# Performance work log

Measured on AMD Instinct MI355X. Metric: run time of the kernel, lower is better.

Reference implementation:

```python
import jax, jax.numpy as jnp
import numpy as np

N_NODES = 128; TIME_DIM = 16; XYZ_DIM = 63; B = 2; V = 1024
_PARAM_SHAPES = {
    'ec1_w': (N_NODES, 72 + TIME_DIM, 64), 'ec1_b': (N_NODES, 64),
    'ec21_w': (N_NODES, 64, 8), 'ec21_b': (N_NODES, 8),
    'ec22_w': (N_NODES, 64, 8), 'ec22_b': (N_NODES, 8),
    'dc1_w': (N_NODES, 80, 64), 'dc1_b': (N_NODES, 64),
    'dc21_w': (N_NODES, 64, 32), 'dc21_b': (N_NODES, 32),
    'dc22_w': (N_NODES, 64, 3), 'dc22_b': (N_NODES, 3),
    'f1_w': (N_NODES, 32 + XYZ_DIM, 64), 'f1_b': (N_NODES, 64),
    'f2_w': (N_NODES, 64, 64), 'f2_b': (N_NODES, 64),
    'f3_w': (N_NODES, 64, 64), 'f3_b': (N_NODES, 64),
    'f4_w': (N_NODES, 64, 256), 'f4_b': (N_NODES, 256),
    'c1_w': (256, 64), 'c1_b': (64,),
    'c2_w': (64, 3), 'c2_b': (3,),
    'd1_w': (256, 1), 'd1_b': (1,),
}
_PNAMES = list(_PARAM_SHAPES.keys())


def setup_inputs():
    key = jax.random.key(0)
    kt, kp, kl, km, kb, kw = jax.random.split(key, 6)
    inp = {
        't_ped': jax.random.normal(kt, (B, TIME_DIM), dtype=jnp.float32),
        'pose': jax.random.normal(kp, (B, 72), dtype=jnp.float32),
        'local_coords': jax.random.normal(kl, (N_NODES, B, V, XYZ_DIM), dtype=jnp.float32),
        'mask': jax.random.randint(km, (N_NODES, B, V), 0, 2) > 0,
        'bweights': jax.random.uniform(kb, (N_NODES, B, V), dtype=jnp.float32),
    }
    for i, (name, shape) in enumerate(_PARAM_SHAPES.items()):
        inp[name] = jax.random.normal(jax.random.fold_in(kw, i), shape, dtype=jnp.float32) * 0.02
    return inp


def _forward(t_ped, pose, local_coords, bweights, mask, p):
    relu = jax.nn.relu
    # ---- encode: 128 per-node Linear(88->64), then ->8 heads (batched as one einsum) ----
    enc_in = jnp.concatenate([t_ped, pose], axis=-1)                                    # [B,88]
    net = relu(jnp.einsum('bi,nio->nbo', enc_in, p['ec1_w']) + p['ec1_b'][:, None, :])  # [n,B,64]
    mean = jnp.einsum('nbi,nio->nbo', net, p['ec21_w']) + p['ec21_b'][:, None, :]       # [n,B,8]
    std = jax.nn.sigmoid(jnp.einsum('nbi,nio->nbo', net, p['ec22_w']) + p['ec22_b'][:, None, :])
    z = mean  # eval mode: z = mean
    # ---- decode: per-node Linear(80->64) then ->32 (ei) and ->3 (delta) ----
    pose_n = jnp.broadcast_to(pose, (N_NODES,) + pose.shape)                            # [n,B,72]
    dec_in = jnp.concatenate([z, pose_n], axis=-1)                                      # [n,B,80]
    dnet = relu(jnp.einsum('nbi,nio->nbo', dec_in, p['dc1_w']) + p['dc1_b'][:, None, :])
    ei = jnp.einsum('nbi,nio->nbo', dnet, p['dc21_w']) + p['dc21_b'][:, None, :]        # [n,B,32]
    nodes_delta = jnp.einsum('nbi,nio->nbo', dnet, p['dc22_w']) + p['dc22_b'][:, None, :]
    # ---- Feature_field: grouped 1x1 conv (groups=128) == per-node MLP; mask/mark
    # pack-unpack in the original is equivalent to dense compute + zeroing non-hits ----
    ei_e = jnp.broadcast_to(ei[:, :, None, :], (N_NODES, B, V, ei.shape[-1]))
    x = jnp.concatenate([ei_e, local_coords], axis=-1)                                  # [n,B,V,95]
    h = relu(jnp.einsum('nbvi,nio->nbvo', x, p['f1_w']) + p['f1_b'][:, None, None, :])
    h = relu(jnp.einsum('nbvi,nio->nbvo', h, p['f2_w']) + p['f2_b'][:, None, None, :])
    h = relu(jnp.einsum('nbvi,nio->nbvo', h, p['f3_w']) + p['f3_b'][:, None, None, :])
    f = relu(jnp.einsum('nbvi,nio->nbvo', h, p['f4_w']) + p['f4_b'][:, None, None, :])  # [n,B,V,256]
    f = jnp.where(mask[..., None], f, jnp.zeros((), f.dtype))                           # f[~mask] = 0
    # ---- blend_feature ----
    bw = jnp.transpose(bweights, (1, 2, 0)) + 1e-7                                      # [B,V,n]
    bw = bw / jnp.sum(bw, axis=-1, keepdims=True)
    f_blend = jnp.einsum('nbvc,bvn->bvc', f, bw)                                        # [B,V,256]
    # ---- Nerf head ----
    netc = relu(f_blend @ p['c1_w'] + p['c1_b'])
    c = netc @ p['c2_w'] + p['c2_b']
    d = relu(f_blend @ p['d1_w'] + p['d1_b'])
    return c, d, ei, nodes_delta, mean, std


def reference(t_ped, pose, local_coords, mask, bweights, ec1_w, ec1_b, ec21_w, ec21_b, ec22_w, ec22_b, dc1_w, dc1_b, dc21_w, dc21_b, dc22_w, dc22_b, f1_w, f1_b, f2_w, f2_b, f3_w, f3_b, f4_w, f4_b, c1_w, c1_b, c2_w, c2_b, d1_w, d1_b):
    p = dict(zip(_PNAMES, (ec1_w, ec1_b, ec21_w, ec21_b, ec22_w, ec22_b, dc1_w, dc1_b, dc21_w, dc21_b, dc22_w, dc22_b, f1_w, f1_b, f2_w, f2_b, f3_w, f3_b, f4_w, f4_b, c1_w, c1_b, c2_w, c2_b, d1_w, d1_b)))
    return _forward(t_ped, pose, local_coords, bweights, mask, p)
```

## Files before the change

### kernel.cpp

```cpp
#include <hip/hip_runtime.h>
#include <hip/hip_bf16.h>
#include <math.h>

typedef __attribute__((ext_vector_type(8))) short short8;
typedef __attribute__((ext_vector_type(4))) float f32x4;

#define W1P_OFF   0u
#define W2P_OFF   1572864u
#define W3P_OFF   2621440u
#define W4P_OFF   3670016u
#define EI_OFF    7864320u
#define RECIP_OFF 7897088u
#define PART_OFF  7905280u

#define OUT_C    0
#define OUT_D    6144
#define OUT_EI   8192
#define OUT_ND   16384
#define OUT_MEAN 17152
#define OUT_STD  19200

__global__ void pack_weights(const float* __restrict__ f1w, const float* __restrict__ f2w,
                             const float* __restrict__ f3w, const float* __restrict__ f4w,
                             __hip_bfloat16* __restrict__ w1p, __hip_bfloat16* __restrict__ w2p,
                             __hip_bfloat16* __restrict__ w3p, __hip_bfloat16* __restrict__ w4p) {
  int id = blockIdx.x * 256 + threadIdx.x;
  union { __hip_bfloat16 h[8]; int4 v; } u;
  if (id < 98304) {
    int n = id / 768, r = id % 768, kc = r >> 6, o = r & 63;
    #pragma unroll
    for (int e = 0; e < 8; e++) {
      int k = kc * 8 + e;
      float val = (k < 95) ? f1w[((size_t)n * 95 + k) * 64 + o] : 0.f;
      u.h[e] = __float2bfloat16(val);
    }
    reinterpret_cast<int4*>(w1p)[id] = u.v;
  } else if (id < 163840) {
    int id2 = id - 98304;
    int n = id2 / 512, r = id2 % 512, kc = r >> 6, o = r & 63;
    #pragma unroll
    for (int e = 0; e < 8; e++)
      u.h[e] = __float2bfloat16(f2w[((size_t)n * 64 + kc * 8 + e) * 64 + o]);
    reinterpret_cast<int4*>(w2p)[id2] = u.v;
  } else if (id < 229376) {
    int id3 = id - 163840;
    int n = id3 / 512, r = id3 % 512, kc = r >> 6, o = r & 63;
    #pragma unroll
    for (int e = 0; e < 8; e++)
      u.h[e] = __float2bfloat16(f3w[((size_t)n * 64 + kc * 8 + e) * 64 + o]);
    reinterpret_cast<int4*>(w3p)[id3] = u.v;
  } else if (id < 491520) {
    int id4 = id - 229376;
    int n = id4 / 2048, r = id4 % 2048, kc = r >> 8, o = r & 255;
    #pragma unroll
    for (int e = 0; e < 8; e++)
      u.h[e] = __float2bfloat16(f4w[((size_t)n * 64 + kc * 8 + e) * 256 + o]);
    reinterpret_cast<int4*>(w4p)[id4] = u.v;
  }
}

__global__ void encdec(const float* __restrict__ t_ped, const float* __restrict__ pose,
                       const float* __restrict__ ec1w, const float* __restrict__ ec1b,
                       const float* __restrict__ ec21w, const float* __restrict__ ec21b,
                       const float* __restrict__ ec22w, const float* __restrict__ ec22b,
                       const float* __restrict__ dc1w, const float* __restrict__ dc1b,
                       const float* __restrict__ dc21w, const float* __restrict__ dc21b,
                       const float* __restrict__ dc22w, const float* __restrict__ dc22b,
                       float* __restrict__ out, float* __restrict__ ei_ws) {
  __shared__ float enc_in[2][88];
  __shared__ float net[2][64];
  __shared__ float dec_in[2][80];
  __shared__ float dnet[2][64];
  int n = blockIdx.x, t = threadIdx.x;
  if (t < 32) { int b = t >> 4, i = t & 15; enc_in[b][i] = t_ped[b * 16 + i]; }
  for (int idx = t; idx < 144; idx += 64) {
    int b = idx / 72, i = idx - b * 72;
    float pv = pose[idx];
    enc_in[b][16 + i] = pv;
    dec_in[b][8 + i] = pv;
  }
  __syncthreads();
  {
    float a0 = ec1b[n * 64 + t], a1 = a0;
    const float* w = ec1w + (size_t)n * 88 * 64 + t;
    for (int i = 0; i < 88; i++) { float wv = w[i * 64]; a0 += enc_in[0][i] * wv; a1 += enc_in[1][i] * wv; }
    net[0][t] = fmaxf(a0, 0.f); net[1][t] = fmaxf(a1, 0.f);
  }
  __syncthreads();
  if (t < 32) {
    int isd = t >> 4, b = (t >> 3) & 1, o = t & 7;
    const float* w = (isd ? ec22w : ec21w) + (size_t)n * 64 * 8 + o;
    float acc = (isd ? ec22b : ec21b)[n * 8 + o];
    for (int i = 0; i < 64; i++) acc += net[b][i] * w[i * 8];
    if (isd) out[OUT_STD + (n * 2 + b) * 8 + o] = 1.f / (1.f + expf(-acc));
    else { out[OUT_MEAN + (n * 2 + b) * 8 + o] = acc; dec_in[b][o] = acc; }
  }
  __syncthreads();
  {
    float a0 = dc1b[n * 64 + t], a1 = a0;
    const float* w = dc1w + (size_t)n * 80 * 64 + t;
    for (int i = 0; i < 80; i++) { float wv = w[i * 64]; a0 += dec_in[0][i] * wv; a1 += dec_in[1][i] * wv; }
    dnet[0][t] = fmaxf(a0, 0.f); dnet[1][t] = fmaxf(a1, 0.f);
  }
  __syncthreads();
  {
    int b = t >> 5, o = t & 31;
    const float* w = dc21w + (size_t)n * 64 * 32 + o;
    float acc = dc21b[n * 32 + o];
    for (int i = 0; i < 64; i++) acc += dnet[b][i] * w[i * 32];
    out[OUT_EI + (n * 2 + b) * 32 + o] = acc;
    ei_ws[(n * 2 + b) * 32 + o] = acc;
  }
  if (t < 6) {
    int b = t / 3, o = t - b * 3;
    const float* w = dc22w + (size_t)n * 64 * 3 + o;
    float acc = dc22b[n * 3 + o];
    for (int i = 0; i < 64; i++) acc += dnet[b][i] * w[i * 3];
    out[OUT_ND + (n * 2 + b) * 3 + o] = acc;
  }
}

__global__ void bwsum(const float* __restrict__ bwt, float* __restrict__ recip) {
  int r = blockIdx.x * 256 + threadIdx.x;
  float s = 0.f;
  for (int n = 0; n < 128; n++) s += bwt[n * 2048 + r];
  recip[r] = 1.f / (s + 128.f * 1e-7f);
}

__launch_bounds__(256, 2)
__global__ void feature_field(const float* __restrict__ coords, const int* __restrict__ mask,
                              const float* __restrict__ bwt,
                              const __hip_bfloat16* __restrict__ w1p, const __hip_bfloat16* __restrict__ w2p,
                              const __hip_bfloat16* __restrict__ w3p, const __hip_bfloat16* __restrict__ w4p,
                              const float* __restrict__ f1b, const float* __restrict__ f2b,
                              const float* __restrict__ f3b, const float* __restrict__ f4b,
                              const float* __restrict__ ei_ws, const float* __restrict__ recip,
                              float* __restrict__ part) {
  __shared__ __align__(16) __hip_bfloat16 xs[64][104];
  __shared__ __align__(16) __hip_bfloat16 hs[2][64][72];
  __shared__ __align__(16) __hip_bfloat16 w1s[12 * 520];
  __shared__ __align__(16) __hip_bfloat16 w23s[2][8 * 520];
  __shared__ float bias_s[448];

  const int tid = threadIdx.x;
  const int g = blockIdx.x >> 5;
  const int tile = blockIdx.x & 31;
  const int b = tile >> 4;
  const int v0 = (tile & 15) << 6;
  const int lane = tid & 63;
  const int wv = tid >> 6;
  const int l16 = lane & 15;
  const int kg = lane >> 4;
  const int arow = wv * 16 + l16;
  const int crow = wv * 16 + kg * 4;

  const f32x4 zero4 = {0.f, 0.f, 0.f, 0.f};
  f32x4 pb[16];
  #pragma unroll
  for (int i = 0; i < 16; i++) pb[i] = zero4;

  for (int ni = 0; ni < 8; ni++) {
    const int n = (g << 3) + ni;
    const float* cb = coords + ((size_t)((n << 1) + b) * 1024 + v0) * 63;
    for (int idx = tid; idx < 4032; idx += 256) {
      int row = idx / 63, c = idx - row * 63;
      xs[row][32 + c] = __float2bfloat16(cb[idx]);
    }
    {
      __hip_bfloat16 eib = __float2bfloat16(ei_ws[((n << 1) + b) * 32 + (tid & 31)]);
      int r0 = tid >> 5;
      #pragma unroll
      for (int k = 0; k < 8; k++) xs[r0 + k * 8][tid & 31] = eib;
    }
    if (tid < 64) {
      #pragma unroll
      for (int c = 95; c < 104; c++) xs[tid][c] = __float2bfloat16(0.f);
    }
    {
      const int4* s1 = reinterpret_cast<const int4*>(w1p + (size_t)n * 6144);
      for (int c = tid; c < 768; c += 256) {
        int kc = c >> 6, o = c & 63;
        *reinterpret_cast<int4*>(&w1s[kc * 520 + o * 8]) = s1[c];
      }
      const int4* s2 = reinterpret_cast<const int4*>(w2p + (size_t)n * 4096);
      const int4* s3 = reinterpret_cast<const int4*>(w3p + (size_t)n * 4096);
      for (int c = tid; c < 512; c += 256) {
        int kc = c >> 6, o = c & 63;
        *reinterpret_cast<int4*>(&w23s[0][kc * 520 + o * 8]) = s2[c];
        *reinterpret_cast<int4*>(&w23s[1][kc * 520 + o * 8]) = s3[c];
      }
      if (tid < 64) bias_s[tid] = f1b[(n << 6) + tid];
      else if (tid < 128) bias_s[tid] = f2b[(n << 6) + tid - 64];
      else if (tid < 192) bias_s[tid] = f3b[(n << 6) + tid - 128];
      bias_s[192 + tid] = f4b[(n << 8) + tid];
    }
    __syncthreads();

    {
      short8 a[3];
      #pragma unroll
      for (int kt = 0; kt < 3; kt++)
        a[kt] = *reinterpret_cast<const short8*>(&xs[arow][kt * 32 + kg * 8]);
      #pragma unroll
      for (int nt = 0; nt < 4; nt++) {
        f32x4 acc = zero4;
        #pragma unroll
        for (int kt = 0; kt < 3; kt++) {
          short8 bf = *reinterpret_cast<const short8*>(&w1s[(kt * 4 + kg) * 520 + (nt * 16 + l16) * 8]);
          acc = __builtin_amdgcn_mfma_f32_16x16x32_bf16(a[kt], bf, acc, 0, 0, 0);
        }
        int col = nt * 16 + l16;
        float bias = bias_s[col];
        #pragma unroll
        for (int r = 0; r < 4; r++)
          hs[0][crow + r][col] = __float2bfloat16(fmaxf(acc[r] + bias, 0.f));
      }
    }
    __syncthreads();
    {
      short8 a[2];
      #pragma unroll
      for (int kt = 0; kt < 2; kt++)
        a[kt] = *reinterpret_cast<const short8*>(&hs[0][arow][kt * 32 + kg * 8]);
      #pragma unroll
      for (int nt = 0; nt < 4; nt++) {
        f32x4 acc = zero4;
        #pragma unroll
        for (int kt = 0; kt < 2; kt++) {
          short8 bf = *reinterpret_cast<const short8*>(&w23s[0][(kt * 4 + kg) * 520 + (nt * 16 + l16) * 8]);
          acc = __builtin_amdgcn_mfma_f32_16x16x32_bf16(a[kt], bf, acc, 0, 0, 0);
        }
        int col = nt * 16 + l16;
        float bias = bias_s[64 + col];
        #pragma unroll
        for (int r = 0; r < 4; r++)
          hs[1][crow + r][col] = __float2bfloat16(fmaxf(acc[r] + bias, 0.f));
      }
    }
    __syncthreads();
    {
      short8 a[2];
      #pragma unroll
      for (int kt = 0; kt < 2; kt++)
        a[kt] = *reinterpret_cast<const short8*>(&hs[1][arow][kt * 32 + kg * 8]);
      #pragma unroll
      for (int nt = 0; nt < 4; nt++) {
        f32x4 acc = zero4;
        #pragma unroll
        for (int kt = 0; kt < 2; kt++) {
          short8 bf = *reinterpret_cast<const short8*>(&w23s[1][(kt * 4 + kg) * 520 + (nt * 16 + l16) * 8]);
          acc = __builtin_amdgcn_mfma_f32_16x16x32_bf16(a[kt], bf, acc, 0, 0, 0);
        }
        int col = nt * 16 + l16;
        float bias = bias_s[128 + col];
        #pragma unroll
        for (int r = 0; r < 4; r++)
          hs[0][crow + r][col] = __float2bfloat16(fmaxf(acc[r] + bias, 0.f));
      }
    }
    __syncthreads();
    {
      short8 a[2];
      #pragma unroll
      for (int kt = 0; kt < 2; kt++)
        a[kt] = *reinterpret_cast<const short8*>(&hs[0][arow][kt * 32 + kg * 8]);
      float wrow[4];
      #pragma unroll
      for (int r = 0; r < 4; r++) {
        int gi = (b << 10) + v0 + crow + r;
        float bwv = (bwt[(n << 11) + gi] + 1e-7f) * recip[gi];
        wrow[r] = (mask[(n << 11) + gi] != 0) ? bwv : 0.f;
      }
      const __hip_bfloat16* w4n = w4p + (size_t)n * 16384;
      #pragma unroll
      for (int nt = 0; nt < 16; nt++) {
        f32x4 acc = zero4;
        #pragma unroll
        for (int kt = 0; kt < 2; kt++) {
          short8 bf = *reinterpret_cast<const short8*>(&w4n[((kt * 4 + kg) * 256 + nt * 16 + l16) * 8]);
          acc = __builtin_amdgcn_mfma_f32_16x16x32_bf16(a[kt], bf, acc, 0, 0, 0);
        }
        float bias = bias_s[192 + nt * 16 + l16];
        #pragma unroll
        for (int r = 0; r < 4; r++) {
          float fv = fmaxf(acc[r] + bias, 0.f);
          pb[nt][r] += wrow[r] * fv;
        }
      }
    }
    __syncthreads();
  }
  {
    const int rbase = (b << 10) + v0 + crow;
    float* pr = part + ((size_t)(g * 2048 + rbase)) * 256 + l16;
    #pragma unroll
    for (int r = 0; r < 4; r++)
      #pragma unroll
      for (int nt = 0; nt < 16; nt++)
        pr[(size_t)r * 256 + nt * 16] = pb[nt][r];
  }
}

__global__ void head(const float* __restrict__ part,
                     const float* __restrict__ c1w, const float* __restrict__ c1b,
                     const float* __restrict__ c2w, const float* __restrict__ c2b,
                     const float* __restrict__ d1w, const float* __restrict__ d1b,
                     float* __restrict__ out) {
  __shared__ float fbs[256];
  __shared__ float ncs[64];
  int row = blockIdx.x;
  int t = threadIdx.x;
  float fb = 0.f;
  for (int gi = 0; gi < 16; gi++) fb += part[((size_t)gi * 2048 + row) * 256 + t];
  fbs[t] = fb;
  __syncthreads();
  if (t < 64) {
    float acc = c1b[t];
    for (int c = 0; c < 256; c++) acc += fbs[c] * c1w[c * 64 + t];
    ncs[t] = fmaxf(acc, 0.f);
  } else if (t >= 192) {
    int l = t - 192;
    float acc = 0.f;
    for (int c = l; c < 256; c += 64) acc += fbs[c] * d1w[c];
    for (int off = 32; off > 0; off >>= 1) acc += __shfl_down(acc, off);
    if (l == 0) out[OUT_D + row] = fmaxf(acc + d1b[0], 0.f);
  }
  __syncthreads();
  if (t < 3) {
    float acc = c2b[t];
    for (int i = 0; i < 64; i++) acc += ncs[i] * c2w[i * 3 + t];
    out[OUT_C + row * 3 + t] = acc;
  }
}

extern "C" void kernel_launch(void* const* d_in, const int* in_sizes, int n_in,
                              void* d_out, int out_size, void* d_ws, size_t ws_size,
                              hipStream_t stream) {
  (void)in_sizes; (void)n_in; (void)out_size; (void)ws_size;
  const float* t_ped  = (const float*)d_in[0];
  const float* pose   = (const float*)d_in[1];
  const float* coords = (const float*)d_in[2];
  const int*   maskp  = (const int*)d_in[3];
  const float* bwt    = (const float*)d_in[4];
  const float* ec1w = (const float*)d_in[5],  *ec1b = (const float*)d_in[6];
  const float* ec21w = (const float*)d_in[7], *ec21b = (const float*)d_in[8];
  const float* ec22w = (const float*)d_in[9], *ec22b = (const float*)d_in[10];
  const float* dc1w = (const float*)d_in[11], *dc1b = (const float*)d_in[12];
  const float* dc21w = (const float*)d_in[13], *dc21b = (const float*)d_in[14];
  const float* dc22w = (const float*)d_in[15], *dc22b = (const float*)d_in[16];
  const float* f1w = (const float*)d_in[17], *f1b = (const float*)d_in[18];
  const float* f2w = (const float*)d_in[19], *f2b = (const float*)d_in[20];
  const float* f3w = (const float*)d_in[21], *f3b = (const float*)d_in[22];
  const float* f4w = (const float*)d_in[23], *f4b = (const float*)d_in[24];
  const float* c1w = (const float*)d_in[25], *c1b = (const float*)d_in[26];
  const float* c2w = (const float*)d_in[27], *c2b = (const float*)d_in[28];
  const float* d1w = (const float*)d_in[29], *d1b = (const float*)d_in[30];
  float* out = (float*)d_out;
  char* ws = (char*)d_ws;
  __hip_bfloat16* w1p = (__hip_bfloat16*)(ws + W1P_OFF);
  __hip_bfloat16* w2p = (__hip_bfloat16*)(ws + W2P_OFF);
  __hip_bfloat16* w3p = (__hip_bfloat16*)(ws + W3P_OFF);
  __hip_bfloat16* w4p = (__hip_bfloat16*)(ws + W4P_OFF);
  float* ei_ws = (float*)(ws + EI_OFF);
  float* recip_ws = (float*)(ws + RECIP_OFF);
  float* part = (float*)(ws + PART_OFF);

  hipLaunchKernelGGL(pack_weights, dim3(1920), dim3(256), 0, stream,
                     f1w, f2w, f3w, f4w, w1p, w2p, w3p, w4p);
  hipLaunchKernelGGL(encdec, dim3(128), dim3(64), 0, stream,
                     t_ped, pose, ec1w, ec1b, ec21w, ec21b, ec22w, ec22b,
                     dc1w, dc1b, dc21w, dc21b, dc22w, dc22b, out, ei_ws);
  hipLaunchKernelGGL(bwsum, dim3(8), dim3(256), 0, stream, bwt, recip_ws);
  hipLaunchKernelGGL(feature_field, dim3(512), dim3(256), 0, stream,
                     coords, maskp, bwt, w1p, w2p, w3p, w4p,
                     f1b, f2b, f3b, f4b, ei_ws, recip_ws, part);
  hipLaunchKernelGGL(head, dim3(2048), dim3(256), 0, stream,
                     part, c1w, c1b, c2w, c2b, d1w, d1b, out);
}
```

Before: 261.0 us.

## Halve feature-field row tile, split output columns across waves, read weights from global

The feature_field kernel now processes 32-vertex tiles instead of 64, doubling the grid. The four waves are arranged as two row tiles by two column halves, so each wave keeps half as many accumulators. The per-node weight and bias staging into LDS is dropped; MFMA B operands and biases are loaded straight from global memory (relying on cache), and coordinate loads use float4. The aim is lower LDS and register use, higher occupancy (launch bounds raised to 4) and less barrier work, at the cost of redundant global/L2 weight traffic per block.

Result: slower. 277.1 us (+6.1%).

```diff
diff --git a/kernel.cpp b/kernel.cpp
--- a/kernel.cpp
+++ b/kernel.cpp
@@ -127,7 +127,7 @@
   recip[r] = 1.f / (s + 128.f * 1e-7f);
 }
 
-__launch_bounds__(256, 2)
+__launch_bounds__(256, 4)
 __global__ void feature_field(const float* __restrict__ coords, const int* __restrict__ mask,
                               const float* __restrict__ bwt,
                               const __hip_bfloat16* __restrict__ w1p, const __hip_bfloat16* __restrict__ w2p,
@@ -136,65 +136,60 @@
                               const float* __restrict__ f3b, const float* __restrict__ f4b,
                               const float* __restrict__ ei_ws, const float* __restrict__ recip,
                               float* __restrict__ part) {
-  __shared__ __align__(16) __hip_bfloat16 xs[64][104];
-  __shared__ __align__(16) __hip_bfloat16 hs[2][64][72];
-  __shared__ __align__(16) __hip_bfloat16 w1s[12 * 520];
-  __shared__ __align__(16) __hip_bfloat16 w23s[2][8 * 520];
-  __shared__ float bias_s[448];
+  __shared__ __align__(16) __hip_bfloat16 xs[32][104];
+  __shared__ __align__(16) __hip_bfloat16 hs[2][32][72];
 
   const int tid = threadIdx.x;
-  const int g = blockIdx.x >> 5;
-  const int tile = blockIdx.x & 31;
-  const int b = tile >> 4;
-  const int v0 = (tile & 15) << 6;
+  const int g = blockIdx.x >> 6;
+  const int tile = blockIdx.x & 63;
+  const int b = tile >> 5;
+  const int v0 = (tile & 31) << 5;
   const int lane = tid & 63;
   const int wv = tid >> 6;
+  const int rt = wv >> 1;
+  const int ch = wv & 1;
   const int l16 = lane & 15;
   const int kg = lane >> 4;
-  const int arow = wv * 16 + l16;
-  const int crow = wv * 16 + kg * 4;
+  const int arow = rt * 16 + l16;
+  const int crow = rt * 16 + kg * 4;
 
   const f32x4 zero4 = {0.f, 0.f, 0.f, 0.f};
-  f32x4 pb[16];
+  f32x4 pb[8];
   #pragma unroll
-  for (int i = 0; i < 16; i++) pb[i] = zero4;
+  for (int i = 0; i < 8; i++) pb[i] = zero4;
+
+  for (int idx = tid; idx < 32 * 9; idx += 256) {
+    int r = idx / 9, c = idx - r * 9;
+    xs[r][95 + c] = __float2bfloat16(0.f);
+  }
 
   for (int ni = 0; ni < 8; ni++) {
     const int n = (g << 3) + ni;
-    const float* cb = coords + ((size_t)((n << 1) + b) * 1024 + v0) * 63;
-    for (int idx = tid; idx < 4032; idx += 256) {
-      int row = idx / 63, c = idx - row * 63;
-      xs[row][32 + c] = __float2bfloat16(cb[idx]);
-    }
-    {
-      __hip_bfloat16 eib = __float2bfloat16(ei_ws[((n << 1) + b) * 32 + (tid & 31)]);
+    {
+      const float* cb = coords + ((size_t)((n << 1) + b) * 1024 + v0) * 63;
+      const float4* cb4 = reinterpret_cast<const float4*>(cb);
+      for (int j = tid; j < 504; j += 256) {
+        float4 v = cb4[j];
+        int idx = j * 4;
+        #pragma unroll
+        for (int e = 0; e < 4; e++) {
+          int ii = idx + e;
+          int row = ii / 63, col = ii - row * 63;
+          xs[row][32 + col] = __float2bfloat16(((const float*)&v)[e]);
+        }
+      }
+      float eif = ei_ws[((n << 1) + b) * 32 + (tid & 31)];
+      __hip_bfloat16 eib = __float2bfloat16(eif);
       int r0 = tid >> 5;
       #pragma unroll
-      for (int k = 0; k < 8; k++) xs[r0 + k * 8][tid & 31] = eib;
-    }
-    if (tid < 64) {
-      #pragma unroll
-      for (int c = 95; c < 104; c++) xs[tid][c] = __float2bfloat16(0.f);
-    }
-    {
-      const int4* s1 = reinterpret_cast<const int4*>(w1p + (size_t)n * 6144);
-      for (int c = tid; c < 768; c += 256) {
-        int kc = c >> 6, o = c & 63;
-        *reinterpret_cast<int4*>(&w1s[kc * 520 + o * 8]) = s1[c];
-      }
-      const int4* s2 = reinterpret_cast<const int4*>(w2p + (size_t)n * 4096);
-      const int4* s3 = reinterpret_cast<const int4*>(w3p + (size_t)n * 4096);
-      for (int c = tid; c < 512; c += 256) {
-        int kc = c >> 6, o = c & 63;
-        *reinterpret_cast<int4*>(&w23s[0][kc * 520 + o * 8]) = s2[c];
-        *reinterpret_cast<int4*>(&w23s[1][kc * 520 + o * 8]) = s3[c];
-      }
-      if (tid < 64) bias_s[tid] = f1b[(n << 6) + tid];
-      else if (tid < 128) bias_s[tid] = f2b[(n << 6) + tid - 64];
-      else if (tid < 192) bias_s[tid] = f3b[(n << 6) + tid - 128];
-      bias_s[192 + tid] = f4b[(n << 8) + tid];
+      for (int k = 0; k < 4; k++) xs[r0 + k * 8][tid & 31] = eib;
     }
     __syncthreads();
+
+    const __hip_bfloat16* w1n = w1p + (size_t)n * 6144;
+    const __hip_bfloat16* w2n = w2p + (size_t)n * 4096;
+    const __hip_bfloat16* w3n = w3p + (size_t)n * 4096;
+    const __hip_bfloat16* w4n = w4p + (size_t)n * 16384;
 
     {
       short8 a[3];
@@ -202,15 +197,16 @@
       for (int kt = 0; kt < 3; kt++)
         a[kt] = *reinterpret_cast<const short8*>(&xs[arow][kt * 32 + kg * 8]);
       #pragma unroll
-      for (int nt = 0; nt < 4; nt++) {
+      for (int nt2 = 0; nt2 < 2; nt2++) {
+        int nt = ch * 2 + nt2;
+        int col = nt * 16 + l16;
         f32x4 acc = zero4;
         #pragma unroll
         for (int kt = 0; kt < 3; kt++) {
-          short8 bf = *reinterpret_cast<const short8*>(&w1s[(kt * 4 + kg) * 520 + (nt * 16 + l16) * 8]);
+          short8 bf = *reinterpret_cast<const short8*>(&w1n[((kt * 4 + kg) * 64 + col) * 8]);
           acc = __builtin_amdgcn_mfma_f32_16x16x32_bf16(a[kt], bf, acc, 0, 0, 0);
         }
-        int col = nt * 16 + l16;
-        float bias = bias_s[col];
+        float bias = f1b[(n << 6) + col];
         #pragma unroll
         for (int r = 0; r < 4; r++)
           hs[0][crow + r][col] = __float2bfloat16(fmaxf(acc[r] + bias, 0.f));
@@ -223,15 +219,16 @@
       for (int kt = 0; kt < 2; kt++)
         a[kt] = *reinterpret_cast<const short8*>(&hs[0][arow][kt * 32 + kg * 8]);
       #pragma unroll
-      for (int nt = 0; nt < 4; nt++) {
+      for (int nt2 = 0; nt2 < 2; nt2++) {
+        int nt = ch * 2 + nt2;
+        int col = nt * 16 + l16;
         f32x4 acc = zero4;
         #pragma unroll
         for (int kt = 0; kt < 2; kt++) {
-          short8 bf = *reinterpret_cast<const short8*>(&w23s[0][(kt * 4 + kg) * 520 + (nt * 16 + l16) * 8]);
+          short8 bf = *reinterpret_cast<const short8*>(&w2n[((kt * 4 + kg) * 64 + col) * 8]);
           acc = __builtin_amdgcn_mfma_f32_16x16x32_bf16(a[kt], bf, acc, 0, 0, 0);
         }
-        int col = nt * 16 + l16;
-        float bias = bias_s[64 + col];
+        float bias = f2b[(n << 6) + col];
         #pragma unroll
         for (int r = 0; r < 4; r++)
           hs[1][crow + r][col] = __float2bfloat16(fmaxf(acc[r] + bias, 0.f));
@@ -244,15 +241,16 @@
       for (int kt = 0; kt < 2; kt++)
         a[kt] = *reinterpret_cast<const short8*>(&hs[1][arow][kt * 32 + kg * 8]);
       #pragma unroll
-      for (int nt = 0; nt < 4; nt++) {
+      for (int nt2 = 0; nt2 < 2; nt2++) {
+        int nt = ch * 2 + nt2;
+        int col = nt * 16 + l16;
         f32x4 acc = zero4;
         #pragma unroll
         for (int kt = 0; kt < 2; kt++) {
-          short8 bf = *reinterpret_cast<const short8*>(&w23s[1][(kt * 4 + kg) * 520 + (nt * 16 + l16) * 8]);
+          short8 bf = *reinterpret_cast<const short8*>(&w3n[((kt * 4 + kg) * 64 + col) * 8]);
           acc = __builtin_amdgcn_mfma_f32_16x16x32_bf16(a[kt], bf, acc, 0, 0, 0);
         }
-        int col = nt * 16 + l16;
-        float bias = bias_s[128 + col];
+        float bias = f3b[(n << 6) + col];
         #pragma unroll
         for (int r = 0; r < 4; r++)
           hs[0][crow + r][col] = __float2bfloat16(fmaxf(acc[r] + bias, 0.f));
@@ -271,24 +269,24 @@
         float bwv = (bwt[(n << 11) + gi] + 1e-7f) * recip[gi];
         wrow[r] = (mask[(n << 11) + gi] != 0) ? bwv : 0.f;
       }
-      const __hip_bfloat16* w4n = w4p + (size_t)n * 16384;
-      #pragma unroll
-      for (int nt = 0; nt < 16; nt++) {
+      #pragma unroll
+      for (int nti = 0; nti < 8; nti++) {
+        int nt = ch * 8 + nti;
+        int col = nt * 16 + l16;
         f32x4 acc = zero4;
         #pragma unroll
         for (int kt = 0; kt < 2; kt++) {
-          short8 bf = *reinterpret_cast<const short8*>(&w4n[((kt * 4 + kg) * 256 + nt * 16 + l16) * 8]);
+          short8 bf = *reinterpret_cast<const short8*>(&w4n[((kt * 4 + kg) * 256 + col) * 8]);
           acc = __builtin_amdgcn_mfma_f32_16x16x32_bf16(a[kt], bf, acc, 0, 0, 0);
         }
-        float bias = bias_s[192 + nt * 16 + l16];
+        float bias = f4b[(n << 8) + col];
         #pragma unroll
         for (int r = 0; r < 4; r++) {
           float fv = fmaxf(acc[r] + bias, 0.f);
-          pb[nt][r] += wrow[r] * fv;
-        }
-      }
-    }
-    __syncthreads();
+          pb[nti][r] += wrow[r] * fv;
+        }
+      }
+    }
   }
   {
     const int rbase = (b << 10) + v0 + crow;
@@ -296,8 +294,8 @@
     #pragma unroll
     for (int r = 0; r < 4; r++)
       #pragma unroll
-      for (int nt = 0; nt < 16; nt++)
-        pr[(size_t)r * 256 + nt * 16] = pb[nt][r];
+      for (int nti = 0; nti < 8; nti++)
+        pr[(size_t)r * 256 + (ch * 8 + nti) * 16] = pb[nti][r];
   }
 }
 
@@ -371,7 +369,7 @@
                      t_ped, pose, ec1w, ec1b, ec21w, ec21b, ec22w, ec22b,
                      dc1w, dc1b, dc21w, dc21b, dc22w, dc22b, out, ei_ws);
   hipLaunchKernelGGL(bwsum, dim3(8), dim3(256), 0, stream, bwt, recip_ws);
-  hipLaunchKernelGGL(feature_field, dim3(512), dim3(256), 0, stream,
+  hipLaunchKernelGGL(feature_field, dim3(1024), dim3(256), 0, stream,
                      coords, maskp, bwt, w1p, w2p, w3p, w4p,
                      f1b, f2b, f3b, f4b, ei_ws, recip_ws, part);
   hipLaunchKernelGGL(head, dim3(2048), dim3(256), 0, stream,
```

## Merge prep kernels and make feature-field waves independent with register-fed MFMA

Applied to the files above, without the earlier changes.

Merges the weight-packing, encoder/decoder and blend-weight-sum kernels into one launch, selecting the role by block index. In the feature-field kernel, each wave now owns its 16 rows end to end. It loads coords and ei directly from global into MFMA A registers and loads packed weights straight from global/L2 into registers instead of staging them in shared memory. Block-wide __syncthreads are replaced by per-wave LDS buffers with wave barriers. This removes block synchronization and LDS staging but adds redundant global weight reads across waves and uncoalesced strided coordinate loads.

Result: faster. 241.1 us (-7.6%).

```diff
diff --git a/kernel.cpp b/kernel.cpp
--- a/kernel.cpp
+++ b/kernel.cpp
@@ -20,111 +20,120 @@
 #define OUT_MEAN 17152
 #define OUT_STD  19200
 
-__global__ void pack_weights(const float* __restrict__ f1w, const float* __restrict__ f2w,
-                             const float* __restrict__ f3w, const float* __restrict__ f4w,
-                             __hip_bfloat16* __restrict__ w1p, __hip_bfloat16* __restrict__ w2p,
-                             __hip_bfloat16* __restrict__ w3p, __hip_bfloat16* __restrict__ w4p) {
-  int id = blockIdx.x * 256 + threadIdx.x;
-  union { __hip_bfloat16 h[8]; int4 v; } u;
-  if (id < 98304) {
-    int n = id / 768, r = id % 768, kc = r >> 6, o = r & 63;
-    #pragma unroll
-    for (int e = 0; e < 8; e++) {
-      int k = kc * 8 + e;
-      float val = (k < 95) ? f1w[((size_t)n * 95 + k) * 64 + o] : 0.f;
-      u.h[e] = __float2bfloat16(val);
-    }
-    reinterpret_cast<int4*>(w1p)[id] = u.v;
-  } else if (id < 163840) {
-    int id2 = id - 98304;
-    int n = id2 / 512, r = id2 % 512, kc = r >> 6, o = r & 63;
-    #pragma unroll
-    for (int e = 0; e < 8; e++)
-      u.h[e] = __float2bfloat16(f2w[((size_t)n * 64 + kc * 8 + e) * 64 + o]);
-    reinterpret_cast<int4*>(w2p)[id2] = u.v;
-  } else if (id < 229376) {
-    int id3 = id - 163840;
-    int n = id3 / 512, r = id3 % 512, kc = r >> 6, o = r & 63;
-    #pragma unroll
-    for (int e = 0; e < 8; e++)
-      u.h[e] = __float2bfloat16(f3w[((size_t)n * 64 + kc * 8 + e) * 64 + o]);
-    reinterpret_cast<int4*>(w3p)[id3] = u.v;
-  } else if (id < 491520) {
-    int id4 = id - 229376;
-    int n = id4 / 2048, r = id4 % 2048, kc = r >> 8, o = r & 255;
-    #pragma unroll
-    for (int e = 0; e < 8; e++)
-      u.h[e] = __float2bfloat16(f4w[((size_t)n * 64 + kc * 8 + e) * 256 + o]);
-    reinterpret_cast<int4*>(w4p)[id4] = u.v;
-  }
-}
-
-__global__ void encdec(const float* __restrict__ t_ped, const float* __restrict__ pose,
-                       const float* __restrict__ ec1w, const float* __restrict__ ec1b,
-                       const float* __restrict__ ec21w, const float* __restrict__ ec21b,
-                       const float* __restrict__ ec22w, const float* __restrict__ ec22b,
-                       const float* __restrict__ dc1w, const float* __restrict__ dc1b,
-                       const float* __restrict__ dc21w, const float* __restrict__ dc21b,
-                       const float* __restrict__ dc22w, const float* __restrict__ dc22b,
-                       float* __restrict__ out, float* __restrict__ ei_ws) {
-  __shared__ float enc_in[2][88];
-  __shared__ float net[2][64];
-  __shared__ float dec_in[2][80];
-  __shared__ float dnet[2][64];
-  int n = blockIdx.x, t = threadIdx.x;
-  if (t < 32) { int b = t >> 4, i = t & 15; enc_in[b][i] = t_ped[b * 16 + i]; }
-  for (int idx = t; idx < 144; idx += 64) {
-    int b = idx / 72, i = idx - b * 72;
-    float pv = pose[idx];
-    enc_in[b][16 + i] = pv;
-    dec_in[b][8 + i] = pv;
-  }
-  __syncthreads();
-  {
-    float a0 = ec1b[n * 64 + t], a1 = a0;
-    const float* w = ec1w + (size_t)n * 88 * 64 + t;
-    for (int i = 0; i < 88; i++) { float wv = w[i * 64]; a0 += enc_in[0][i] * wv; a1 += enc_in[1][i] * wv; }
-    net[0][t] = fmaxf(a0, 0.f); net[1][t] = fmaxf(a1, 0.f);
-  }
-  __syncthreads();
-  if (t < 32) {
-    int isd = t >> 4, b = (t >> 3) & 1, o = t & 7;
-    const float* w = (isd ? ec22w : ec21w) + (size_t)n * 64 * 8 + o;
-    float acc = (isd ? ec22b : ec21b)[n * 8 + o];
-    for (int i = 0; i < 64; i++) acc += net[b][i] * w[i * 8];
-    if (isd) out[OUT_STD + (n * 2 + b) * 8 + o] = 1.f / (1.f + expf(-acc));
-    else { out[OUT_MEAN + (n * 2 + b) * 8 + o] = acc; dec_in[b][o] = acc; }
-  }
-  __syncthreads();
-  {
-    float a0 = dc1b[n * 64 + t], a1 = a0;
-    const float* w = dc1w + (size_t)n * 80 * 64 + t;
-    for (int i = 0; i < 80; i++) { float wv = w[i * 64]; a0 += dec_in[0][i] * wv; a1 += dec_in[1][i] * wv; }
-    dnet[0][t] = fmaxf(a0, 0.f); dnet[1][t] = fmaxf(a1, 0.f);
-  }
-  __syncthreads();
-  {
-    int b = t >> 5, o = t & 31;
-    const float* w = dc21w + (size_t)n * 64 * 32 + o;
-    float acc = dc21b[n * 32 + o];
-    for (int i = 0; i < 64; i++) acc += dnet[b][i] * w[i * 32];
-    out[OUT_EI + (n * 2 + b) * 32 + o] = acc;
-    ei_ws[(n * 2 + b) * 32 + o] = acc;
-  }
-  if (t < 6) {
-    int b = t / 3, o = t - b * 3;
-    const float* w = dc22w + (size_t)n * 64 * 3 + o;
-    float acc = dc22b[n * 3 + o];
-    for (int i = 0; i < 64; i++) acc += dnet[b][i] * w[i * 3];
-    out[OUT_ND + (n * 2 + b) * 3 + o] = acc;
-  }
-}
-
-__global__ void bwsum(const float* __restrict__ bwt, float* __restrict__ recip) {
-  int r = blockIdx.x * 256 + threadIdx.x;
-  float s = 0.f;
-  for (int n = 0; n < 128; n++) s += bwt[n * 2048 + r];
-  recip[r] = 1.f / (s + 128.f * 1e-7f);
+__device__ __forceinline__ short f2bs(float x) {
+  __hip_bfloat16 h = __float2bfloat16(x);
+  union { __hip_bfloat16 hh; short s; } u; u.hh = h; return u.s;
+}
+
+__global__ void prep(const float* __restrict__ f1w, const float* __restrict__ f2w,
+                     const float* __restrict__ f3w, const float* __restrict__ f4w,
+                     __hip_bfloat16* __restrict__ w1p, __hip_bfloat16* __restrict__ w2p,
+                     __hip_bfloat16* __restrict__ w3p, __hip_bfloat16* __restrict__ w4p,
+                     const float* __restrict__ t_ped, const float* __restrict__ pose,
+                     const float* __restrict__ ec1w, const float* __restrict__ ec1b,
+                     const float* __restrict__ ec21w, const float* __restrict__ ec21b,
+                     const float* __restrict__ ec22w, const float* __restrict__ ec22b,
+                     const float* __restrict__ dc1w, const float* __restrict__ dc1b,
+                     const float* __restrict__ dc21w, const float* __restrict__ dc21b,
+                     const float* __restrict__ dc22w, const float* __restrict__ dc22b,
+                     const float* __restrict__ bwt,
+                     float* __restrict__ out, float* __restrict__ ei_ws,
+                     float* __restrict__ recip) {
+  const int bid = blockIdx.x;
+  const int tid = threadIdx.x;
+  if (bid < 1920) {
+    int id = bid * 256 + tid;
+    union { __hip_bfloat16 h[8]; int4 v; } u;
+    if (id < 98304) {
+      int n = id / 768, r = id % 768, kc = r >> 6, o = r & 63;
+      #pragma unroll
+      for (int e = 0; e < 8; e++) {
+        int k = kc * 8 + e;
+        float val = (k < 95) ? f1w[((size_t)n * 95 + k) * 64 + o] : 0.f;
+        u.h[e] = __float2bfloat16(val);
+      }
+      reinterpret_cast<int4*>(w1p)[id] = u.v;
+    } else if (id < 163840) {
+      int id2 = id - 98304;
+      int n = id2 / 512, r = id2 % 512, kc = r >> 6, o = r & 63;
+      #pragma unroll
+      for (int e = 0; e < 8; e++)
+        u.h[e] = __float2bfloat16(f2w[((size_t)n * 64 + kc * 8 + e) * 64 + o]);
+      reinterpret_cast<int4*>(w2p)[id2] = u.v;
+    } else if (id < 229376) {
+      int id3 = id - 163840;
+      int n = id3 / 512, r = id3 % 512, kc = r >> 6, o = r & 63;
+      #pragma unroll
+      for (int e = 0; e < 8; e++)
+        u.h[e] = __float2bfloat16(f3w[((size_t)n * 64 + kc * 8 + e) * 64 + o]);
+      reinterpret_cast<int4*>(w3p)[id3] = u.v;
+    } else {
+      int id4 = id - 229376;
+      int n = id4 / 2048, r = id4 % 2048, kc = r >> 8, o = r & 255;
+      #pragma unroll
+      for (int e = 0; e < 8; e++)
+        u.h[e] = __float2bfloat16(f4w[((size_t)n * 64 + kc * 8 + e) * 256 + o]);
+      reinterpret_cast<int4*>(w4p)[id4] = u.v;
+    }
+  } else if (bid < 1952) {
+    __shared__ float enc_in[4][2][88];
+    __shared__ float net[4][2][64];
+    __shared__ float dec_in[4][2][80];
+    __shared__ float dnet[4][2][64];
+    const int sub = tid >> 6, t = tid & 63;
+    const int n = (bid - 1920) * 4 + sub;
+    if (t < 32) { int b = t >> 4, i = t & 15; enc_in[sub][b][i] = t_ped[b * 16 + i]; }
+    for (int idx = t; idx < 144; idx += 64) {
+      int b = idx / 72, i = idx - b * 72;
+      float pv = pose[idx];
+      enc_in[sub][b][16 + i] = pv;
+      dec_in[sub][b][8 + i] = pv;
+    }
+    __syncthreads();
+    {
+      float a0 = ec1b[n * 64 + t], a1 = a0;
+      const float* w = ec1w + (size_t)n * 88 * 64 + t;
+      for (int i = 0; i < 88; i++) { float wv = w[i * 64]; a0 += enc_in[sub][0][i] * wv; a1 += enc_in[sub][1][i] * wv; }
+      net[sub][0][t] = fmaxf(a0, 0.f); net[sub][1][t] = fmaxf(a1, 0.f);
+    }
+    __syncthreads();
+    if (t < 32) {
+      int isd = t >> 4, b = (t >> 3) & 1, o = t & 7;
+      const float* w = (isd ? ec22w : ec21w) + (size_t)n * 64 * 8 + o;
+      float acc = (isd ? ec22b : ec21b)[n * 8 + o];
+      for (int i = 0; i < 64; i++) acc += net[sub][b][i] * w[i * 8];
+      if (isd) out[OUT_STD + (n * 2 + b) * 8 + o] = 1.f / (1.f + expf(-acc));
+      else { out[OUT_MEAN + (n * 2 + b) * 8 + o] = acc; dec_in[sub][b][o] = acc; }
+    }
+    __syncthreads();
+    {
+      float a0 = dc1b[n * 64 + t], a1 = a0;
+      const float* w = dc1w + (size_t)n * 80 * 64 + t;
+      for (int i = 0; i < 80; i++) { float wv = w[i * 64]; a0 += dec_in[sub][0][i] * wv; a1 += dec_in[sub][1][i] * wv; }
+      dnet[sub][0][t] = fmaxf(a0, 0.f); dnet[sub][1][t] = fmaxf(a1, 0.f);
+    }
+    __syncthreads();
+    {
+      int b = t >> 5, o = t & 31;
+      const float* w = dc21w + (size_t)n * 64 * 32 + o;
+      float acc = dc21b[n * 32 + o];
+      for (int i = 0; i < 64; i++) acc += dnet[sub][b][i] * w[i * 32];
+      out[OUT_EI + (n * 2 + b) * 32 + o] = acc;
+      ei_ws[(n * 2 + b) * 32 + o] = acc;
+    }
+    if (t < 6) {
+      int b = t / 3, o = t - b * 3;
+      const float* w = dc22w + (size_t)n * 64 * 3 + o;
+      float acc = dc22b[n * 3 + o];
+      for (int i = 0; i < 64; i++) acc += dnet[sub][b][i] * w[i * 3];
+      out[OUT_ND + (n * 2 + b) * 3 + o] = acc;
+    }
+  } else {
+    int r = (bid - 1952) * 256 + tid;
+    float s = 0.f;
+    for (int n = 0; n < 128; n++) s += bwt[n * 2048 + r];
+    recip[r] = 1.f / (s + 128.f * 1e-7f);
+  }
 }
 
 __launch_bounds__(256, 2)
@@ -136,23 +145,17 @@
                               const float* __restrict__ f3b, const float* __restrict__ f4b,
                               const float* __restrict__ ei_ws, const float* __restrict__ recip,
                               float* __restrict__ part) {
-  __shared__ __align__(16) __hip_bfloat16 xs[64][104];
-  __shared__ __align__(16) __hip_bfloat16 hs[2][64][72];
-  __shared__ __align__(16) __hip_bfloat16 w1s[12 * 520];
-  __shared__ __align__(16) __hip_bfloat16 w23s[2][8 * 520];
-  __shared__ float bias_s[448];
+  __shared__ __align__(16) __hip_bfloat16 hbuf[4][16][72];
 
   const int tid = threadIdx.x;
-  const int g = blockIdx.x >> 5;
-  const int tile = blockIdx.x & 31;
-  const int b = tile >> 4;
-  const int v0 = (tile & 15) << 6;
+  const int wv = tid >> 6;
   const int lane = tid & 63;
-  const int wv = tid >> 6;
   const int l16 = lane & 15;
   const int kg = lane >> 4;
-  const int arow = wv * 16 + l16;
-  const int crow = wv * 16 + kg * 4;
+  const int g = blockIdx.x >> 5;
+  const int row0 = (blockIdx.x & 31) * 64 + wv * 16;
+  const int b = row0 >> 10;
+  const int v0 = row0 & 1023;
 
   const f32x4 zero4 = {0.f, 0.f, 0.f, 0.f};
   f32x4 pb[16];
@@ -161,138 +164,139 @@
 
   for (int ni = 0; ni < 8; ni++) {
     const int n = (g << 3) + ni;
-    const float* cb = coords + ((size_t)((n << 1) + b) * 1024 + v0) * 63;
-    for (int idx = tid; idx < 4032; idx += 256) {
-      int row = idx / 63, c = idx - row * 63;
-      xs[row][32 + c] = __float2bfloat16(cb[idx]);
-    }
-    {
-      __hip_bfloat16 eib = __float2bfloat16(ei_ws[((n << 1) + b) * 32 + (tid & 31)]);
-      int r0 = tid >> 5;
-      #pragma unroll
-      for (int k = 0; k < 8; k++) xs[r0 + k * 8][tid & 31] = eib;
-    }
-    if (tid < 64) {
-      #pragma unroll
-      for (int c = 95; c < 104; c++) xs[tid][c] = __float2bfloat16(0.f);
-    }
-    {
-      const int4* s1 = reinterpret_cast<const int4*>(w1p + (size_t)n * 6144);
-      for (int c = tid; c < 768; c += 256) {
-        int kc = c >> 6, o = c & 63;
-        *reinterpret_cast<int4*>(&w1s[kc * 520 + o * 8]) = s1[c];
-      }
-      const int4* s2 = reinterpret_cast<const int4*>(w2p + (size_t)n * 4096);
-      const int4* s3 = reinterpret_cast<const int4*>(w3p + (size_t)n * 4096);
-      for (int c = tid; c < 512; c += 256) {
-        int kc = c >> 6, o = c & 63;
-        *reinterpret_cast<int4*>(&w23s[0][kc * 520 + o * 8]) = s2[c];
-        *reinterpret_cast<int4*>(&w23s[1][kc * 520 + o * 8]) = s3[c];
-      }
-      if (tid < 64) bias_s[tid] = f1b[(n << 6) + tid];
-      else if (tid < 128) bias_s[tid] = f2b[(n << 6) + tid - 64];
-      else if (tid < 192) bias_s[tid] = f3b[(n << 6) + tid - 128];
-      bias_s[192 + tid] = f4b[(n << 8) + tid];
-    }
-    __syncthreads();
-
-    {
-      short8 a[3];
-      #pragma unroll
-      for (int kt = 0; kt < 3; kt++)
-        a[kt] = *reinterpret_cast<const short8*>(&xs[arow][kt * 32 + kg * 8]);
+    short8 a0, a1, a2;
+    {
+      const float* ep = ei_ws + ((n << 1) + b) * 32 + kg * 8;
+      #pragma unroll
+      for (int e = 0; e < 8; e++) a0[e] = f2bs(ep[e]);
+      const float* cp = coords + ((size_t)((n << 1) + b) * 1024 + v0 + l16) * 63;
+      #pragma unroll
+      for (int e = 0; e < 8; e++) a1[e] = f2bs(cp[kg * 8 + e]);
+      #pragma unroll
+      for (int e = 0; e < 8; e++) {
+        int c = 32 + kg * 8 + e;
+        a2[e] = (c < 63) ? f2bs(cp[c]) : (short)0;
+      }
+    }
+    const __hip_bfloat16* w1n = w1p + (size_t)n * 6144;
+    const __hip_bfloat16* w2n = w2p + (size_t)n * 4096;
+    const __hip_bfloat16* w3n = w3p + (size_t)n * 4096;
+    const __hip_bfloat16* w4n = w4p + (size_t)n * 16384;
+
+    {
+      short8 bf[12];
+      #pragma unroll
+      for (int nt = 0; nt < 4; nt++)
+        #pragma unroll
+        for (int kt = 0; kt < 3; kt++)
+          bf[nt * 3 + kt] = *reinterpret_cast<const short8*>(&w1n[((kt * 4 + kg) * 64 + nt * 16 + l16) * 8]);
       #pragma unroll
       for (int nt = 0; nt < 4; nt++) {
         f32x4 acc = zero4;
-        #pragma unroll
-        for (int kt = 0; kt < 3; kt++) {
-          short8 bf = *reinterpret_cast<const short8*>(&w1s[(kt * 4 + kg) * 520 + (nt * 16 + l16) * 8]);
-          acc = __builtin_amdgcn_mfma_f32_16x16x32_bf16(a[kt], bf, acc, 0, 0, 0);
-        }
+        acc = __builtin_amdgcn_mfma_f32_16x16x32_bf16(a0, bf[nt * 3 + 0], acc, 0, 0, 0);
+        acc = __builtin_amdgcn_mfma_f32_16x16x32_bf16(a1, bf[nt * 3 + 1], acc, 0, 0, 0);
+        acc = __builtin_amdgcn_mfma_f32_16x16x32_bf16(a2, bf[nt * 3 + 2], acc, 0, 0, 0);
         int col = nt * 16 + l16;
-        float bias = bias_s[col];
+        float bias = f1b[(n << 6) + col];
         #pragma unroll
         for (int r = 0; r < 4; r++)
-          hs[0][crow + r][col] = __float2bfloat16(fmaxf(acc[r] + bias, 0.f));
-      }
-    }
-    __syncthreads();
-    {
-      short8 a[2];
+          hbuf[wv][kg * 4 + r][col] = __float2bfloat16(fmaxf(acc[r] + bias, 0.f));
+      }
+    }
+    asm volatile("s_waitcnt lgkmcnt(0)");
+    __builtin_amdgcn_wave_barrier();
+    {
+      short8 ha[2];
       #pragma unroll
       for (int kt = 0; kt < 2; kt++)
-        a[kt] = *reinterpret_cast<const short8*>(&hs[0][arow][kt * 32 + kg * 8]);
+        ha[kt] = *reinterpret_cast<const short8*>(&hbuf[wv][l16][kt * 32 + kg * 8]);
+      __builtin_amdgcn_wave_barrier();
+      short8 bf[8];
+      #pragma unroll
+      for (int nt = 0; nt < 4; nt++)
+        #pragma unroll
+        for (int kt = 0; kt < 2; kt++)
+          bf[nt * 2 + kt] = *reinterpret_cast<const short8*>(&w2n[((kt * 4 + kg) * 64 + nt * 16 + l16) * 8]);
       #pragma unroll
       for (int nt = 0; nt < 4; nt++) {
         f32x4 acc = zero4;
-        #pragma unroll
-        for (int kt = 0; kt < 2; kt++) {
-          short8 bf = *reinterpret_cast<const short8*>(&w23s[0][(kt * 4 + kg) * 520 + (nt * 16 + l16) * 8]);
-          acc = __builtin_amdgcn_mfma_f32_16x16x32_bf16(a[kt], bf, acc, 0, 0, 0);
-        }
+        acc = __builtin_amdgcn_mfma_f32_16x16x32_bf16(ha[0], bf[nt * 2 + 0], acc, 0, 0, 0);
+        acc = __builtin_amdgcn_mfma_f32_16x16x32_bf16(ha[1], bf[nt * 2 + 1], acc, 0, 0, 0);
         int col = nt * 16 + l16;
-        float bias = bias_s[64 + col];
+        float bias = f2b[(n << 6) + col];
         #pragma unroll
         for (int r = 0; r < 4; r++)
-          hs[1][crow + r][col] = __float2bfloat16(fmaxf(acc[r] + bias, 0.f));
-      }
-    }
-    __syncthreads();
-    {
-      short8 a[2];
+          hbuf[wv][kg * 4 + r][col] = __float2bfloat16(fmaxf(acc[r] + bias, 0.f));
+      }
+    }
+    asm volatile("s_waitcnt lgkmcnt(0)");
+    __builtin_amdgcn_wave_barrier();
+    {
+      short8 ha[2];
       #pragma unroll
       for (int kt = 0; kt < 2; kt++)
-        a[kt] = *reinterpret_cast<const short8*>(&hs[1][arow][kt * 32 + kg * 8]);
+        ha[kt] = *reinterpret_cast<const short8*>(&hbuf[wv][l16][kt * 32 + kg * 8]);
+      __builtin_amdgcn_wave_barrier();
+      short8 bf[8];
+      #pragma unroll
+      for (int nt = 0; nt < 4; nt++)
+        #pragma unroll
+        for (int kt = 0; kt < 2; kt++)
+          bf[nt * 2 + kt] = *reinterpret_cast<const short8*>(&w3n[((kt * 4 + kg) * 64 + nt * 16 + l16) * 8]);
       #pragma unroll
       for (int nt = 0; nt < 4; nt++) {
         f32x4 acc = zero4;
-        #pragma unroll
-        for (int kt = 0; kt < 2; kt++) {
-          short8 bf = *reinterpret_cast<const short8*>(&w23s[1][(kt * 4 + kg) * 520 + (nt * 16 + l16) * 8]);
-          acc = __builtin_amdgcn_mfma_f32_16x16x32_bf16(a[kt], bf, acc, 0, 0, 0);
-        }
+        acc = __builtin_amdgcn_mfma_f32_16x16x32_bf16(ha[0], bf[nt * 2 + 0], acc, 0, 0, 0);
+        acc = __builtin_amdgcn_mfma_f32_16x16x32_bf16(ha[1], bf[nt * 2 + 1], acc, 0, 0, 0);
         int col = nt * 16 + l16;
-        float bias = bias_s[128 + col];
+        float bias = f3b[(n << 6) + col];
         #pragma unroll
         for (int r = 0; r < 4; r++)
-          hs[0][crow + r][col] = __float2bfloat16(fmaxf(acc[r] + bias, 0.f));
-      }
-    }
-    __syncthreads();
-    {
-      short8 a[2];
+          hbuf[wv][kg * 4 + r][col] = __float2bfloat16(fmaxf(acc[r] + bias, 0.f));
+      }
+    }
+    asm volatile("s_waitcnt lgkmcnt(0)");
+    __builtin_amdgcn_wave_barrier();
+    {
+      short8 ha[2];
       #pragma unroll
       for (int kt = 0; kt < 2; kt++)
-        a[kt] = *reinterpret_cast<const short8*>(&hs[0][arow][kt * 32 + kg * 8]);
+        ha[kt] = *reinterpret_cast<const short8*>(&hbuf[wv][l16][kt * 32 + kg * 8]);
+      __builtin_amdgcn_wave_barrier();
       float wrow[4];
       #pragma unroll
       for (int r = 0; r < 4; r++) {
-        int gi = (b << 10) + v0 + crow + r;
+        int gi = row0 + kg * 4 + r;
         float bwv = (bwt[(n << 11) + gi] + 1e-7f) * recip[gi];
         wrow[r] = (mask[(n << 11) + gi] != 0) ? bwv : 0.f;
       }
-      const __hip_bfloat16* w4n = w4p + (size_t)n * 16384;
-      #pragma unroll
-      for (int nt = 0; nt < 16; nt++) {
-        f32x4 acc = zero4;
-        #pragma unroll
-        for (int kt = 0; kt < 2; kt++) {
-          short8 bf = *reinterpret_cast<const short8*>(&w4n[((kt * 4 + kg) * 256 + nt * 16 + l16) * 8]);
-          acc = __builtin_amdgcn_mfma_f32_16x16x32_bf16(a[kt], bf, acc, 0, 0, 0);
+      #pragma unroll
+      for (int c = 0; c < 4; c++) {
+        short8 bf[8];
+        #pragma unroll
+        for (int nti = 0; nti < 4; nti++)
+          #pragma unroll
+          for (int kt = 0; kt < 2; kt++)
+            bf[nti * 2 + kt] = *reinterpret_cast<const short8*>(&w4n[((kt * 4 + kg) * 256 + (c * 4 + nti) * 16 + l16) * 8]);
+        #pragma unroll
+        for (int nti = 0; nti < 4; nti++) {
+          f32x4 acc = zero4;
+          acc = __builtin_amdgcn_mfma_f32_16x16x32_bf16(ha[0], bf[nti * 2 + 0], acc, 0, 0, 0);
+          acc = __builtin_amdgcn_mfma_f32_16x16x32_bf16(ha[1], bf[nti * 2 + 1], acc, 0, 0, 0);
+          int nt = c * 4 + nti;
+          float bias = f4b[(n << 8) + nt * 16 + l16];
+          #pragma unroll
+          for (int r = 0; r < 4; r++) {
+            float fv = fmaxf(acc[r] + bias, 0.f);
+            pb[nt][r] += wrow[r] * fv;
+          }
         }
-        float bias = bias_s[192 + nt * 16 + l16];
-        #pragma unroll
-        for (int r = 0; r < 4; r++) {
-          float fv = fmaxf(acc[r] + bias, 0.f);
-          pb[nt][r] += wrow[r] * fv;
-        }
-      }
-    }
-    __syncthreads();
+      }
+    }
+    __builtin_amdgcn_wave_barrier();
   }
   {
-    const int rbase = (b << 10) + v0 + crow;
-    float* pr = part + ((size_t)(g * 2048 + rbase)) * 256 + l16;
+    float* pr = part + ((size_t)(g * 2048 + row0 + kg * 4)) * 256 + l16;
     #pragma unroll
     for (int r = 0; r < 4; r++)
       #pragma unroll
@@ -365,12 +369,11 @@
   float* recip_ws = (float*)(ws + RECIP_OFF);
   float* part = (float*)(ws + PART_OFF);
 
-  hipLaunchKernelGGL(pack_weights, dim3(1920), dim3(256), 0, stream,
-                     f1w, f2w, f3w, f4w, w1p, w2p, w3p, w4p);
-  hipLaunchKernelGGL(encdec, dim3(128), dim3(64), 0, stream,
+  hipLaunchKernelGGL(prep, dim3(1960), dim3(256), 0, stream,
+                     f1w, f2w, f3w, f4w, w1p, w2p, w3p, w4p,
                      t_ped, pose, ec1w, ec1b, ec21w, ec21b, ec22w, ec22b,
-                     dc1w, dc1b, dc21w, dc21b, dc22w, dc22b, out, ei_ws);
-  hipLaunchKernelGGL(bwsum, dim3(8), dim3(256), 0, stream, bwt, recip_ws);
+                     dc1w, dc1b, dc21w, dc21b, dc22w, dc22b,
+                     bwt, out, ei_ws, recip_ws);
   hipLaunchKernelGGL(feature_field, dim3(512), dim3(256), 0, stream,
                      coords, maskp, bwt, w1p, w2p, w3p, w4p,
                      f1b, f2b, f3b, f4b, ei_ws, recip_ws, part);
```
